# Performance work log

Measured on AMD Instinct MI355X. Metric: run time of the kernel, lower is better.

Reference implementation:

```python
import jax, jax.numpy as jnp
import numpy as np

B, L, D = 16, 4096, 1024          # batch, query (latent) length, latent_dim
MODS = [("image", 2048), ("audio", 1024), ("text", 768)]


def setup_inputs() -> dict:
    key = jax.random.key(0)
    ks = iter(jax.random.split(key, 64))
    inp = {"S": jax.random.normal(next(ks), (B, L, D), jnp.float32)}
    for mod, din in MODS:
        inp[f"feat_{mod}"] = jax.random.normal(next(ks), (B, din), jnp.float32)
        # kv_proj: Linear(input_dim -> latent_dim)
        inp[f"Wkv_{mod}"] = jax.random.normal(next(ks), (D, din), jnp.float32) * (din ** -0.5)
        inp[f"bkv_{mod}"] = jnp.zeros((D,), jnp.float32)
        # MHA value projection (D -> D); k/q projections drop out because
        # softmax over a single key is identically 1 (exact, not approximate).
        inp[f"Wv_{mod}"] = jax.random.normal(next(ks), (D, D), jnp.float32) * (D ** -0.5)
        inp[f"bv_{mod}"] = jnp.zeros((D,), jnp.float32)
        # MHA out_proj (D -> D)
        inp[f"Wo_{mod}"] = jax.random.normal(next(ks), (D, D), jnp.float32) * (D ** -0.5)
        inp[f"bo_{mod}"] = jnp.zeros((D,), jnp.float32)
    return inp


def _modality_out(feat, Wkv, bkv, Wv, bv, Wo, bo):
    # kv_proj -> v_proj -> out_proj ; attention weights over 1 key are exactly 1,
    # so the MHA output is this vector broadcast over all L query positions.
    kv = feat @ Wkv.T + bkv        # [B, D]
    v = kv @ Wv.T + bv             # [B, D]
    return v @ Wo.T + bo           # [B, D]


def reference(S,
              feat_image, Wkv_image, bkv_image, Wv_image, bv_image, Wo_image, bo_image,
              feat_audio, Wkv_audio, bkv_audio, Wv_audio, bv_audio, Wo_audio, bo_audio,
              feat_text, Wkv_text, bkv_text, Wv_text, bv_text, Wo_text, bo_text):
    # Sequential residual adds S = S + out_mod commute; fuse into one add.
    delta = (_modality_out(feat_image, Wkv_image, bkv_image, Wv_image, bv_image, Wo_image, bo_image)
             + _modality_out(feat_audio, Wkv_audio, bkv_audio, Wv_audio, bv_audio, Wo_audio, bo_audio)
             + _modality_out(feat_text, Wkv_text, bkv_text, Wv_text, bv_text, Wo_text, bo_text))
    return S + delta[:, None, :]   # broadcast over query length L
```

## Files before the change

### kernel.cpp

```cpp
#include <hip/hip_runtime.h>


#define B_ 16
#define L_ 4096
#define D_ 1024

typedef float v4f __attribute__((ext_vector_type(4)));

struct StageArgs {
    const float* x[3];
    const float* W[3];
    const float* bias[3];
    float*       y[3];
    int          K[3];
};

__global__ __launch_bounds__(256) void gemv_stage(StageArgs a) {
    int wid  = (blockIdx.x * 256 + threadIdx.x) >> 6;
    int lane = threadIdx.x & 63;
    int m = wid >> 14;
    int r = wid & 16383;
    int bb = r >> 10;
    int d  = r & 1023;
    int K = a.K[m];

    const float* xr = a.x[m] + bb * K;
    const float* wr = a.W[m] + (size_t)d * K;

    float sum = 0.f;
    for (int k = lane * 4; k < K; k += 256) {
        float4 xv = *(const float4*)(xr + k);
        float4 wv = *(const float4*)(wr + k);
        sum += xv.x * wv.x + xv.y * wv.y + xv.z * wv.z + xv.w * wv.w;
    }
    for (int off = 32; off; off >>= 1) sum += __shfl_xor(sum, off, 64);

    if (lane == 0) a.y[m][(bb << 10) + d] = sum + a.bias[m][d];
}

struct Stage3Args {
    const float* v0; const float* v1; const float* v2;
    const float* W0; const float* W1; const float* W2;
    const float* b0; const float* b1; const float* b2;
    float* delta;
};

__global__ __launch_bounds__(256) void gemv_stage3(Stage3Args a) {
    int wid  = (blockIdx.x * 256 + threadIdx.x) >> 6;
    int lane = threadIdx.x & 63;
    int bb = wid >> 10;
    int d  = wid & 1023;

    const float* xs[3] = { a.v0 + (bb << 10), a.v1 + (bb << 10), a.v2 + (bb << 10) };
    const float* ws[3] = { a.W0 + ((size_t)d << 10), a.W1 + ((size_t)d << 10),
                           a.W2 + ((size_t)d << 10) };
    float sum = 0.f;
    #pragma unroll
    for (int m = 0; m < 3; ++m) {
        const float* xr = xs[m];
        const float* wr = ws[m];
        #pragma unroll
        for (int k = lane * 4; k < 1024; k += 256) {
            float4 xv = *(const float4*)(xr + k);
            float4 wv = *(const float4*)(wr + k);
            sum += xv.x * wv.x + xv.y * wv.y + xv.z * wv.z + xv.w * wv.w;
        }
    }
    for (int off = 32; off; off >>= 1) sum += __shfl_xor(sum, off, 64);

    if (lane == 0)
        a.delta[(bb << 10) + d] = sum + a.b0[d] + a.b1[d] + a.b2[d];
}

__global__ __launch_bounds__(256) void add_bcast(const v4f* __restrict__ S,
                                                 const v4f* __restrict__ delta,
                                                 v4f* __restrict__ out) {
    int tid   = blockIdx.x * 256 + threadIdx.x;
    int d4    = tid & 255;
    int chunk = (tid >> 8) & 127;
    int b     = tid >> 15;

    v4f dl = delta[(b << 8) + d4];

    size_t base = ((size_t)b << 20) + ((size_t)chunk << 13) + (size_t)d4;

    #pragma unroll 8
    for (int j = 0; j < 32; ++j) {
        size_t idx = base + ((size_t)j << 8);
        v4f s = __builtin_nontemporal_load(S + idx);
        __builtin_nontemporal_store(s + dl, out + idx);
    }
}

extern "C" void kernel_launch(void* const* d_in, const int* in_sizes, int n_in,
                              void* d_out, int out_size, void* d_ws, size_t ws_size,
                              hipStream_t stream) {
    const float* S = (const float*)d_in[0];

    const int dins[3] = {2048, 1024, 768};
    const float *feat[3], *Wkv[3], *bkv[3], *Wv[3], *bv[3], *Wo[3], *bo[3];
    for (int m = 0; m < 3; ++m) {
        int base = 1 + m * 7;
        feat[m] = (const float*)d_in[base + 0];
        Wkv[m]  = (const float*)d_in[base + 1];
        bkv[m]  = (const float*)d_in[base + 2];
        Wv[m]   = (const float*)d_in[base + 3];
        bv[m]   = (const float*)d_in[base + 4];
        Wo[m]   = (const float*)d_in[base + 5];
        bo[m]   = (const float*)d_in[base + 6];
    }

    float* ws = (float*)d_ws;
    const int BD = B_ * D_;
    float* kv[3]  = {ws, ws + BD, ws + 2 * BD};
    float* v[3]   = {ws + 3 * BD, ws + 4 * BD, ws + 5 * BD};
    float* delta  = ws + 6 * BD;

    StageArgs s1;
    for (int m = 0; m < 3; ++m) {
        s1.x[m] = feat[m]; s1.W[m] = Wkv[m]; s1.bias[m] = bkv[m];
        s1.y[m] = kv[m];   s1.K[m] = dins[m];
    }
    gemv_stage<<<12288, 256, 0, stream>>>(s1);

    StageArgs s2;
    for (int m = 0; m < 3; ++m) {
        s2.x[m] = kv[m]; s2.W[m] = Wv[m]; s2.bias[m] = bv[m];
        s2.y[m] = v[m];  s2.K[m] = D_;
    }
    gemv_stage<<<12288, 256, 0, stream>>>(s2);

    Stage3Args s3 = { v[0], v[1], v[2], Wo[0], Wo[1], Wo[2], bo[0], bo[1], bo[2], delta };
    gemv_stage3<<<4096, 256, 0, stream>>>(s3);

    add_bcast<<<2048, 256, 0, stream>>>((const v4f*)S, (const v4f*)delta,
                                        (v4f*)d_out);
}
```

Baseline: 541.1 us.

## Compute all 16 batch rows per wave to reuse each weight row load

Each wave of the three GEMV stages now computes one output feature for all 16 batch rows, so every weight row is read once instead of once per batch. The activations, which are small and likely cache-resident, are reloaded per batch inside the loop. This removes the redundant weight traffic of the batch-per-wave mapping. In exchange it cuts the grids to 768 and 256 blocks and adds 16 accumulators per thread plus 16 separate shuffle reductions, which lowers parallelism and may raise register pressure.

```diff
diff --git a/kernel.cpp b/kernel.cpp
--- a/kernel.cpp
+++ b/kernel.cpp
@@ -7,7 +7,7 @@
 
 typedef float v4f __attribute__((ext_vector_type(4)));
 
-struct StageArgs {
+struct AllBArgs {
     const float* x[3];
     const float* W[3];
     const float* bias[3];
@@ -15,27 +15,36 @@
     int          K[3];
 };
 
-__global__ __launch_bounds__(256) void gemv_stage(StageArgs a) {
+__global__ __launch_bounds__(256) void gemv_allb(AllBArgs a) {
     int wid  = (blockIdx.x * 256 + threadIdx.x) >> 6;
     int lane = threadIdx.x & 63;
-    int m = wid >> 14;
-    int r = wid & 16383;
-    int bb = r >> 10;
-    int d  = r & 1023;
+    int m = wid >> 10;
+    int d = wid & 1023;
     int K = a.K[m];
 
-    const float* xr = a.x[m] + bb * K;
     const float* wr = a.W[m] + (size_t)d * K;
+    const float* xb = a.x[m];
 
-    float sum = 0.f;
+    float sum[16];
+    #pragma unroll
+    for (int b = 0; b < 16; ++b) sum[b] = 0.f;
+
     for (int k = lane * 4; k < K; k += 256) {
-        float4 xv = *(const float4*)(xr + k);
         float4 wv = *(const float4*)(wr + k);
-        sum += xv.x * wv.x + xv.y * wv.y + xv.z * wv.z + xv.w * wv.w;
+        #pragma unroll
+        for (int b = 0; b < 16; ++b) {
+            float4 xv = *(const float4*)(xb + b * K + k);
+            sum[b] += xv.x * wv.x + xv.y * wv.y + xv.z * wv.z + xv.w * wv.w;
+        }
     }
-    for (int off = 32; off; off >>= 1) sum += __shfl_xor(sum, off, 64);
 
-    if (lane == 0) a.y[m][(bb << 10) + d] = sum + a.bias[m][d];
+    float bias = a.bias[m][d];
+    #pragma unroll
+    for (int b = 0; b < 16; ++b) {
+        float s = sum[b];
+        for (int off = 32; off; off >>= 1) s += __shfl_xor(s, off, 64);
+        if (lane == 0) a.y[m][(b << 10) + d] = s + bias;
+    }
 }
 
 struct Stage3Args {
@@ -45,31 +54,41 @@
     float* delta;
 };
 
-__global__ __launch_bounds__(256) void gemv_stage3(Stage3Args a) {
+__global__ __launch_bounds__(256) void gemv3_allb(Stage3Args a) {
     int wid  = (blockIdx.x * 256 + threadIdx.x) >> 6;
     int lane = threadIdx.x & 63;
-    int bb = wid >> 10;
-    int d  = wid & 1023;
+    int d = wid & 1023;
 
-    const float* xs[3] = { a.v0 + (bb << 10), a.v1 + (bb << 10), a.v2 + (bb << 10) };
+    const float* xs[3] = { a.v0, a.v1, a.v2 };
     const float* ws[3] = { a.W0 + ((size_t)d << 10), a.W1 + ((size_t)d << 10),
                            a.W2 + ((size_t)d << 10) };
-    float sum = 0.f;
+
+    float sum[16];
+    #pragma unroll
+    for (int b = 0; b < 16; ++b) sum[b] = 0.f;
+
     #pragma unroll
     for (int m = 0; m < 3; ++m) {
-        const float* xr = xs[m];
         const float* wr = ws[m];
+        const float* xb = xs[m];
         #pragma unroll
         for (int k = lane * 4; k < 1024; k += 256) {
-            float4 xv = *(const float4*)(xr + k);
             float4 wv = *(const float4*)(wr + k);
-            sum += xv.x * wv.x + xv.y * wv.y + xv.z * wv.z + xv.w * wv.w;
+            #pragma unroll
+            for (int b = 0; b < 16; ++b) {
+                float4 xv = *(const float4*)(xb + (b << 10) + k);
+                sum[b] += xv.x * wv.x + xv.y * wv.y + xv.z * wv.z + xv.w * wv.w;
+            }
         }
     }
-    for (int off = 32; off; off >>= 1) sum += __shfl_xor(sum, off, 64);
 
-    if (lane == 0)
-        a.delta[(bb << 10) + d] = sum + a.b0[d] + a.b1[d] + a.b2[d];
+    float bias = a.b0[d] + a.b1[d] + a.b2[d];
+    #pragma unroll
+    for (int b = 0; b < 16; ++b) {
+        float s = sum[b];
+        for (int off = 32; off; off >>= 1) s += __shfl_xor(s, off, 64);
+        if (lane == 0) a.delta[(b << 10) + d] = s + bias;
+    }
 }
 
 __global__ __launch_bounds__(256) void add_bcast(const v4f* __restrict__ S,
@@ -116,22 +135,22 @@
     float* v[3]   = {ws + 3 * BD, ws + 4 * BD, ws + 5 * BD};
     float* delta  = ws + 6 * BD;
 
-    StageArgs s1;
+    AllBArgs s1;
     for (int m = 0; m < 3; ++m) {
         s1.x[m] = feat[m]; s1.W[m] = Wkv[m]; s1.bias[m] = bkv[m];
         s1.y[m] = kv[m];   s1.K[m] = dins[m];
     }
-    gemv_stage<<<12288, 256, 0, stream>>>(s1);
+    gemv_allb<<<768, 256, 0, stream>>>(s1);
 
-    StageArgs s2;
+    AllBArgs s2;
     for (int m = 0; m < 3; ++m) {
         s2.x[m] = kv[m]; s2.W[m] = Wv[m]; s2.bias[m] = bv[m];
         s2.y[m] = v[m];  s2.K[m] = D_;
     }
-    gemv_stage<<<12288, 256, 0, stream>>>(s2);
+    gemv_allb<<<768, 256, 0, stream>>>(s2);
 
     Stage3Args s3 = { v[0], v[1], v[2], Wo[0], Wo[1], Wo[2], bo[0], bo[1], bo[2], delta };
-    gemv_stage3<<<4096, 256, 0, stream>>>(s3);
+    gemv3_allb<<<256, 256, 0, stream>>>(s3);
 
     add_bcast<<<2048, 256, 0, stream>>>((const v4f*)S, (const v4f*)delta,
                                         (v4f*)d_out);
```

Measured after the change: 567.7 us. +4.9%, slower.
